# Optimization experiments

Hardware: AMD Instinct MI355X
Metric: run time of the kernel (lower is better)

Reference implementation:

```python
import jax, jax.numpy as jnp
import numpy as np

Q = 200000       # number of logical qubits
C = 64           # number of cores
D = 128          # core_emb_shape == d_E == d_H


def setup_inputs() -> dict:
    key = jax.random.key(0)
    k1, k2, k3, k4, k5, k6 = jax.random.split(key, 6)
    prev_assign = jax.random.randint(k1, (Q,), 0, C)
    q_embeddings = jax.random.normal(k2, (Q, D), dtype=jnp.float32)
    padding_emb = jnp.zeros((D,), dtype=jnp.float32)
    # symmetric 0/1 core connectivity matrix
    a = (jax.random.uniform(k3, (C, C)) < 0.3).astype(jnp.float32)
    core_con = jnp.maximum(a, a.T) * (1.0 - jnp.eye(C, dtype=jnp.float32))
    # single GNN layer params: relu(X Wself + A X Wmsg + b)
    W_self = jax.random.normal(k4, (D, D), dtype=jnp.float32) / np.sqrt(D)
    W_msg = jax.random.normal(k5, (D, D), dtype=jnp.float32) / np.sqrt(D)
    b = jax.random.normal(k6, (D,), dtype=jnp.float32) * 0.01
    return {"prev_assign": prev_assign, "q_embeddings": q_embeddings,
            "padding_emb": padding_emb, "core_con": core_con,
            "W_self": W_self, "W_msg": W_msg, "b": b}


def reference(prev_assign, q_embeddings, padding_emb, core_con, W_self, W_msg, b):
    n_cores = core_con.shape[0]
    # fused per-core max-reduce over qubit embeddings grouped by prev_assign
    seg_max = jax.ops.segment_max(q_embeddings, prev_assign, num_segments=n_cores)  # [C, D]
    counts = jax.ops.segment_sum(jnp.ones((q_embeddings.shape[0],), q_embeddings.dtype),
                                 prev_assign, num_segments=n_cores)                 # [C]
    core_embs = jnp.where((counts > 0)[:, None], seg_max, padding_emb[None, :])     # [C, D]
    # GNN over core connectivity graph (single message-passing layer)
    msg = core_con @ (core_embs @ W_msg)            # [C, D]
    return jax.nn.relu(core_embs @ W_self + msg + b)  # [C, D]
```

## Files before the change

kernel.cpp:

```cpp
#include <hip/hip_runtime.h>
#include <math.h>

#define D 128
#define C 64
#define P1_THREADS 1024
#define P1_GRID 256

__device__ __forceinline__ unsigned f2key(float f) {
  unsigned u = __float_as_uint(f);
  return (u & 0x80000000u) ? ~u : (u | 0x80000000u);
}
__device__ __forceinline__ float key2f(unsigned k) {
  unsigned u = (k & 0x80000000u) ? (k & 0x7fffffffu) : ~k;
  return __uint_as_float(u);
}

__global__ __launch_bounds__(P1_THREADS) void p1_segmax(
    const int* __restrict__ assign, const float* __restrict__ qe,
    unsigned* __restrict__ part, int Q, int niter) {
  __shared__ unsigned buf[C * D];
  int tid = threadIdx.x;
  for (int i = tid; i < C * D; i += P1_THREADS) buf[i] = 0u;
  __syncthreads();

  int lane = tid & 31;
  int r = tid >> 5;

  for (int it = blockIdx.x; it < niter; it += gridDim.x) {
    int base = it * 128;
    if (base + 128 <= Q) {
      float4 v[4];
      int a[4];
#pragma unroll
      for (int i = 0; i < 4; ++i) {
        int row = base + i * 32 + r;
        v[i] = *(const float4*)&qe[(size_t)row * D + lane * 4];
        a[i] = assign[row] * D + lane;
      }
#pragma unroll
      for (int i = 0; i < 4; ++i) {
        atomicMax(&buf[a[i] +  0], f2key(v[i].x));
        atomicMax(&buf[a[i] + 32], f2key(v[i].y));
        atomicMax(&buf[a[i] + 64], f2key(v[i].z));
        atomicMax(&buf[a[i] + 96], f2key(v[i].w));
      }
    } else {
      for (int i = 0; i < 4; ++i) {
        int row = base + i * 32 + r;
        if (row < Q) {
          float4 v = *(const float4*)&qe[(size_t)row * D + lane * 4];
          int a = assign[row] * D + lane;
          atomicMax(&buf[a +  0], f2key(v.x));
          atomicMax(&buf[a + 32], f2key(v.y));
          atomicMax(&buf[a + 64], f2key(v.z));
          atomicMax(&buf[a + 96], f2key(v.w));
        }
      }
    }
  }
  __syncthreads();

  unsigned* outp = part + (size_t)blockIdx.x * (C * D);
  for (int i = tid; i < C * D; i += P1_THREADS) {
    int d = i & 127;
    outp[i] = buf[(i & ~127) + (d & 3) * 32 + (d >> 2)];
  }
}

__global__ __launch_bounds__(256) void p2_merge(
    const unsigned* __restrict__ part, const float* __restrict__ padding,
    float* __restrict__ core_embs, int nb) {
  __shared__ unsigned red[256];
  int tid = threadIdx.x;
  int o = blockIdx.x * 32 + (tid & 31);
  int rdr = tid >> 5;
  unsigned m = 0u;
#pragma unroll 8
  for (int br = rdr; br < nb; br += 8)
    m = max(m, part[(size_t)br * (C * D) + o]);
  red[tid] = m;
  __syncthreads();
  if (tid < 32) {
    unsigned k = m;
#pragma unroll
    for (int j = 1; j < 8; ++j) k = max(k, red[j * 32 + tid]);
    core_embs[o] = k ? key2f(k) : padding[o & (D - 1)];
  }
}

__global__ __launch_bounds__(D) void p3_fused(
    const float* __restrict__ core_embs, const float* __restrict__ con,
    const float* __restrict__ Wself, const float* __restrict__ Wmsg,
    const float* __restrict__ b, float* __restrict__ out) {
  __shared__ float CE[C * D];
  __shared__ float Mrow[D];
  __shared__ float crow[C];
  int t = threadIdx.x;
  int c = blockIdx.x;
  for (int i = t; i < C * D; i += D) CE[i] = core_embs[i];
  if (t < C) crow[t] = con[c * C + t];
  __syncthreads();
  float m = 0.f;
#pragma unroll 8
  for (int j = 0; j < C; ++j) m += crow[j] * CE[j * D + t];
  Mrow[t] = m;
  __syncthreads();
  float acc = b[t];
#pragma unroll 8
  for (int k = 0; k < D; ++k) acc += CE[c * D + k] * Wself[k * D + t];
#pragma unroll 8
  for (int k = 0; k < D; ++k) acc += Mrow[k] * Wmsg[k * D + t];
  out[c * D + t] = fmaxf(acc, 0.f);
}

extern "C" void kernel_launch(void* const* d_in, const int* in_sizes, int n_in,
                              void* d_out, int out_size, void* d_ws, size_t ws_size,
                              hipStream_t stream) {
  const int* assign    = (const int*)d_in[0];
  const float* qe      = (const float*)d_in[1];
  const float* padding = (const float*)d_in[2];
  const float* con     = (const float*)d_in[3];
  const float* Wself   = (const float*)d_in[4];
  const float* Wmsg    = (const float*)d_in[5];
  const float* b       = (const float*)d_in[6];
  float* out = (float*)d_out;
  int Q = in_sizes[0];

  const size_t slot = (size_t)C * D;
  size_t avail = ws_size / 4;
  long nb_max = (long)((avail > slot ? avail - slot : slot) / slot);
  int nb = (int)(nb_max < P1_GRID ? nb_max : P1_GRID);
  if (nb < 1) nb = 1;

  unsigned* part   = (unsigned*)d_ws;
  float* core_embs = (float*)((unsigned*)d_ws + (size_t)nb * slot);

  int niter = (Q + 127) / 128;

  hipLaunchKernelGGL(p1_segmax, dim3(nb), dim3(P1_THREADS), 0, stream,
                     assign, qe, part, Q, niter);
  hipLaunchKernelGGL(p2_merge, dim3((C * D) / 32), dim3(256), 0, stream,
                     part, padding, core_embs, nb);
  hipLaunchKernelGGL(p3_fused, dim3(C), dim3(D), 0, stream,
                     core_embs, con, Wself, Wmsg, b, out);
}
```

Before: 182.9 us.

## Prefetch next tile in segmax, vectorize merge, split-K the GNN kernel

The segment-max kernel now double-buffers its loop. It issues the global loads for the next 128-row tile before doing the shared-memory atomics on the current one, so memory latency overlaps the atomics. Tail rows are clamped to the last row instead of taking a separate branch, which is safe because max is idempotent. The merge kernel reads the partials as uint4 with one block per core, which means fewer and wider loads but also fewer blocks. The GNN kernel splits both the message sum and the K reduction across two 128-thread halves and reads core embeddings from global memory. It also adds rows only where the connectivity entry is nonzero, which assumes the matrix holds only 0/1 values.

```diff
diff --git a/kernel.cpp b/kernel.cpp
--- a/kernel.cpp
+++ b/kernel.cpp
@@ -15,48 +15,62 @@
   return __uint_as_float(u);
 }
 
+
+__device__ __forceinline__ void p1_load(const int* __restrict__ assign,
+                                        const float* __restrict__ qe, int Q,
+                                        int base, int lane, int r,
+                                        float4* v, int* a) {
+#pragma unroll
+  for (int i = 0; i < 4; ++i) {
+    int row = base + i * 32 + r;
+    row = row < Q ? row : Q - 1;
+    v[i] = *(const float4*)&qe[(size_t)row * D + lane * 4];
+    a[i] = assign[row] * D + lane;
+  }
+}
+
+__device__ __forceinline__ void p1_atom(unsigned* buf, const float4* v,
+                                        const int* a) {
+#pragma unroll
+  for (int i = 0; i < 4; ++i) {
+    atomicMax(&buf[a[i] +  0], f2key(v[i].x));
+    atomicMax(&buf[a[i] + 32], f2key(v[i].y));
+    atomicMax(&buf[a[i] + 64], f2key(v[i].z));
+    atomicMax(&buf[a[i] + 96], f2key(v[i].w));
+  }
+}
+
 __global__ __launch_bounds__(P1_THREADS) void p1_segmax(
     const int* __restrict__ assign, const float* __restrict__ qe,
     unsigned* __restrict__ part, int Q, int niter) {
   __shared__ unsigned buf[C * D];
   int tid = threadIdx.x;
   for (int i = tid; i < C * D; i += P1_THREADS) buf[i] = 0u;
-  __syncthreads();
 
   int lane = tid & 31;
   int r = tid >> 5;
+  int stride = gridDim.x;
 
-  for (int it = blockIdx.x; it < niter; it += gridDim.x) {
-    int base = it * 128;
-    if (base + 128 <= Q) {
-      float4 v[4];
-      int a[4];
+  int it = blockIdx.x;
+  bool any = it < niter;
+  float4 v0[4];
+  int a0[4];
+  if (any) p1_load(assign, qe, Q, it * 128, lane, r, v0, a0);
+  __syncthreads();
+
+  while (any) {
+    int nx = it + stride;
+    bool more = nx < niter;
+    float4 v1[4];
+    int a1[4];
+    if (more) p1_load(assign, qe, Q, nx * 128, lane, r, v1, a1);
+    p1_atom(buf, v0, a0);
+    if (more) {
 #pragma unroll
-      for (int i = 0; i < 4; ++i) {
-        int row = base + i * 32 + r;
-        v[i] = *(const float4*)&qe[(size_t)row * D + lane * 4];
-        a[i] = assign[row] * D + lane;
-      }
-#pragma unroll
-      for (int i = 0; i < 4; ++i) {
-        atomicMax(&buf[a[i] +  0], f2key(v[i].x));
-        atomicMax(&buf[a[i] + 32], f2key(v[i].y));
-        atomicMax(&buf[a[i] + 64], f2key(v[i].z));
-        atomicMax(&buf[a[i] + 96], f2key(v[i].w));
-      }
-    } else {
-      for (int i = 0; i < 4; ++i) {
-        int row = base + i * 32 + r;
-        if (row < Q) {
-          float4 v = *(const float4*)&qe[(size_t)row * D + lane * 4];
-          int a = assign[row] * D + lane;
-          atomicMax(&buf[a +  0], f2key(v.x));
-          atomicMax(&buf[a + 32], f2key(v.y));
-          atomicMax(&buf[a + 64], f2key(v.z));
-          atomicMax(&buf[a + 96], f2key(v.w));
-        }
-      }
+      for (int i = 0; i < 4; ++i) { v0[i] = v1[i]; a0[i] = a1[i]; }
     }
+    it = nx;
+    any = more;
   }
   __syncthreads();
 
@@ -70,47 +84,83 @@
 __global__ __launch_bounds__(256) void p2_merge(
     const unsigned* __restrict__ part, const float* __restrict__ padding,
     float* __restrict__ core_embs, int nb) {
-  __shared__ unsigned red[256];
+  __shared__ uint4 red[8][32];
   int tid = threadIdx.x;
-  int o = blockIdx.x * 32 + (tid & 31);
+  int q = tid & 31;
   int rdr = tid >> 5;
-  unsigned m = 0u;
+  int c = blockIdx.x;
+  size_t base = (size_t)c * D + q * 4;
+
+  uint4 m = make_uint4(0u, 0u, 0u, 0u);
 #pragma unroll 8
-  for (int br = rdr; br < nb; br += 8)
-    m = max(m, part[(size_t)br * (C * D) + o]);
-  red[tid] = m;
+  for (int br = rdr; br < nb; br += 8) {
+    uint4 x = *(const uint4*)(part + (size_t)br * (C * D) + base);
+    m.x = max(m.x, x.x);
+    m.y = max(m.y, x.y);
+    m.z = max(m.z, x.z);
+    m.w = max(m.w, x.w);
+  }
+  red[rdr][q] = m;
   __syncthreads();
   if (tid < 32) {
-    unsigned k = m;
+    uint4 k = red[0][tid];
 #pragma unroll
-    for (int j = 1; j < 8; ++j) k = max(k, red[j * 32 + tid]);
-    core_embs[o] = k ? key2f(k) : padding[o & (D - 1)];
+    for (int j = 1; j < 8; ++j) {
+      uint4 x = red[j][tid];
+      k.x = max(k.x, x.x);
+      k.y = max(k.y, x.y);
+      k.z = max(k.z, x.z);
+      k.w = max(k.w, x.w);
+    }
+    float4 o;
+    o.x = k.x ? key2f(k.x) : padding[tid * 4 + 0];
+    o.y = k.y ? key2f(k.y) : padding[tid * 4 + 1];
+    o.z = k.z ? key2f(k.z) : padding[tid * 4 + 2];
+    o.w = k.w ? key2f(k.w) : padding[tid * 4 + 3];
+    *(float4*)(core_embs + (size_t)c * D + tid * 4) = o;
   }
 }
 
-__global__ __launch_bounds__(D) void p3_fused(
+__global__ __launch_bounds__(256) void p3_fused(
     const float* __restrict__ core_embs, const float* __restrict__ con,
     const float* __restrict__ Wself, const float* __restrict__ Wmsg,
     const float* __restrict__ b, float* __restrict__ out) {
-  __shared__ float CE[C * D];
-  __shared__ float Mrow[D];
   __shared__ float crow[C];
-  int t = threadIdx.x;
+  __shared__ float CEc[D];
+  __shared__ float Mp[2][D];
+  __shared__ float Ap[2][D];
+  int tid = threadIdx.x;
   int c = blockIdx.x;
-  for (int i = t; i < C * D; i += D) CE[i] = core_embs[i];
-  if (t < C) crow[t] = con[c * C + t];
+  int t = tid & (D - 1);
+  int h = tid >> 7;
+
+  if (tid < C) crow[tid] = con[c * C + tid];
+  if (tid < D) CEc[tid] = core_embs[(size_t)c * D + tid];
   __syncthreads();
+
   float m = 0.f;
+  int j0 = h * 32;
+#pragma unroll
+  for (int jj = 0; jj < 32; ++jj) {
+    int j = j0 + jj;
+    if (crow[j] != 0.f)
+      m += core_embs[(size_t)j * D + t];
+  }
+  Mp[h][t] = m;
+  __syncthreads();
+
+  float acc = (h == 0) ? b[t] : 0.f;
+  int k0 = h * 64;
 #pragma unroll 8
-  for (int j = 0; j < C; ++j) m += crow[j] * CE[j * D + t];
-  Mrow[t] = m;
+  for (int kk = 0; kk < 64; ++kk) {
+    int k = k0 + kk;
+    float mr = Mp[0][k] + Mp[1][k];
+    acc = fmaf(CEc[k], Wself[(size_t)k * D + t], acc);
+    acc = fmaf(mr, Wmsg[(size_t)k * D + t], acc);
+  }
+  Ap[h][t] = acc;
   __syncthreads();
-  float acc = b[t];
-#pragma unroll 8
-  for (int k = 0; k < D; ++k) acc += CE[c * D + k] * Wself[k * D + t];
-#pragma unroll 8
-  for (int k = 0; k < D; ++k) acc += Mrow[k] * Wmsg[k * D + t];
-  out[c * D + t] = fmaxf(acc, 0.f);
+  if (h == 0) out[(size_t)c * D + t] = fmaxf(Ap[0][t] + Ap[1][t], 0.f);
 }
 
 extern "C" void kernel_launch(void* const* d_in, const int* in_sizes, int n_in,
@@ -139,8 +189,8 @@
 
   hipLaunchKernelGGL(p1_segmax, dim3(nb), dim3(P1_THREADS), 0, stream,
                      assign, qe, part, Q, niter);
-  hipLaunchKernelGGL(p2_merge, dim3((C * D) / 32), dim3(256), 0, stream,
+  hipLaunchKernelGGL(p2_merge, dim3(C), dim3(256), 0, stream,
                      part, padding, core_embs, nb);
-  hipLaunchKernelGGL(p3_fused, dim3(C), dim3(D), 0, stream,
+  hipLaunchKernelGGL(p3_fused, dim3(C), dim3(256), 0, stream,
                      core_embs, con, Wself, Wmsg, b, out);
 }
```

Measured after the change: 183.1 us. Within noise of the previous version (+0.1%).
